# Performance work log

Measured on AMD Instinct MI355X. Metric: run time of the kernel, lower is better.

## Reference

```python
import jax, jax.numpy as jnp
import numpy as np

B, F, C_IN, C_OUT, W_DIM, K2, PAD = 4, 98304, 256, 3, 512, 4, 4096
N = B * F  # total real faces across batch


def setup_inputs() -> dict:
    key = jax.random.key(0)
    ks = jax.random.split(key, 5)
    x = jax.random.normal(ks[0], (N, C_IN), jnp.float32)
    face_neighborhood = jax.random.randint(ks[1], (N, K2), 0, N + PAD)
    # pads placed at the end of the padded slot array (exactly PAD true entries)
    face_is_pad = jnp.concatenate([jnp.zeros((N,), bool), jnp.ones((PAD,), bool)])
    w = jax.random.normal(ks[2], (B, W_DIM), jnp.float32)
    affine_weight = jax.random.normal(ks[3], (C_IN, W_DIM), jnp.float32)
    affine_bias = jnp.ones((C_IN,), jnp.float32)  # bias_init=1
    weight = jax.random.normal(ks[4], (C_OUT, C_IN, 1, K2), jnp.float32)
    bias = jnp.zeros((C_OUT,), jnp.float32)
    return dict(x=x, face_neighborhood=face_neighborhood, face_is_pad=face_is_pad,
                pad_size=PAD, w=w, affine_weight=affine_weight,
                affine_bias=affine_bias, weight=weight, bias=bias)


def reference(x, face_neighborhood, face_is_pad, pad_size, w,
              affine_weight, affine_bias, weight, bias):
    weight_gain = 1.0 / np.sqrt(C_IN * K2)
    # FullyConnectedLayer (stylegan2-ada): out = w @ (A.T / sqrt(in)) + bias(=1)
    styles = (w @ (affine_weight.T / np.float32(np.sqrt(W_DIM))) + affine_bias) * weight_gain  # [B, C_in]
    # create_faceconv_input: scatter real features into padded slots (pads = 0)
    real_rank = jnp.cumsum(~face_is_pad) - 1                      # [N+pad] rank among real slots
    padded = jnp.where(face_is_pad[:, None], jnp.float32(0),
                       x[jnp.clip(real_rank, 0, N - 1)])           # [N+pad, C_in]
    gathered = padded[face_neighborhood]                           # [N, K2, C_in]
    g = gathered.reshape(B, F, K2, C_IN)
    # modulated_face_conv, demodulate=False:
    # out[b,f,o] = sum_{c,k} g[b,f,k,c] * weight[o,c,0,k] * styles[b,c]
    out = jnp.einsum('bfkc,ock,bc->bfo', g, weight[:, :, 0, :], styles)
    out = out.reshape(N, C_OUT) + bias[None, :]
    return jnp.clip(out, -256.0, 256.0)
```

## Files before the change

kernel.cpp:

```cpp
#include <hip/hip_runtime.h>


#define N_FACES   393216
#define C_IN      256
#define C_OUT     3
#define W_DIM     512
#define K2        4
#define BATCH     4
#define F_PER_B   98304
#define NJ        48

typedef __attribute__((ext_vector_type(8))) short bf16x8;
typedef __attribute__((ext_vector_type(4))) float f32x4;

static __device__ __forceinline__ unsigned short f2bf(float f) {
    union { float f; unsigned int u; } v; v.f = f;
    unsigned int r = v.u + 0x7FFFu + ((v.u >> 16) & 1u);
    return (unsigned short)(r >> 16);
}
static __device__ __forceinline__ float bf2f(unsigned short u) {
    union { unsigned int u; float f; } v; v.u = ((unsigned int)u) << 16;
    return v.f;
}

__global__ __launch_bounds__(256) void wmod_bf16_kernel(
    const float* __restrict__ w,
    const float* __restrict__ aw,
    const float* __restrict__ ab,
    const float* __restrict__ weight,
    unsigned short* __restrict__ wmodT)
{
    int t = blockIdx.x * blockDim.x + threadIdx.x;
    if (t >= BATCH * C_IN) return;
    int b = t >> 8;
    int c = t & 255;

    const float* wr = w  + b * W_DIM;
    const float* ar = aw + c * W_DIM;
    float acc = 0.f;
    #pragma unroll 4
    for (int d = 0; d < W_DIM; d += 4) {
        float4 wv = *reinterpret_cast<const float4*>(wr + d);
        float4 av = *reinterpret_cast<const float4*>(ar + d);
        acc += wv.x * av.x + wv.y * av.y + wv.z * av.z + wv.w * av.w;
    }
    const float rsqrt_wdim = 0.04419417382415922f;
    const float gain       = 0.03125f;
    float s = (acc * rsqrt_wdim + ab[c]) * gain;

    #pragma unroll
    for (int o = 0; o < C_OUT; ++o)
        #pragma unroll
        for (int k = 0; k < K2; ++k) {
            int j = b * (K2 * C_OUT) + k * C_OUT + o;
            wmodT[j * C_IN + c] = f2bf(weight[(o * C_IN + c) * K2 + k] * s);
        }
}

#define LDW (C_IN + 8)

__global__ __launch_bounds__(256) void gemm_z_kernel(
    const float*          __restrict__ x,
    const unsigned short* __restrict__ wmodT,
    unsigned short*       __restrict__ z)
{
    __shared__ unsigned short bs[NJ][LDW];

    const unsigned int* g = reinterpret_cast<const unsigned int*>(wmodT);
    for (int i = threadIdx.x; i < NJ * (C_IN / 2); i += 256) {
        int r = i >> 7;
        int c = i & 127;
        reinterpret_cast<unsigned int*>(&bs[r][0])[c] = g[r * 128 + c];
    }
    __syncthreads();

    const int tile = (blockIdx.x * 256 + threadIdx.x) >> 6;
    const int lane = threadIdx.x & 63;
    const int row  = lane & 15;
    const int kq   = lane >> 4;

    const float* xrow = x + (size_t)(tile * 16 + row) * C_IN + kq * 8;

    f32x4 acc0 = {0.f, 0.f, 0.f, 0.f};
    f32x4 acc1 = {0.f, 0.f, 0.f, 0.f};
    f32x4 acc2 = {0.f, 0.f, 0.f, 0.f};

    #pragma unroll
    for (int ks = 0; ks < 8; ++ks) {
        const float4* p = reinterpret_cast<const float4*>(xrow + ks * 32);
        float4 a0 = p[0];
        float4 a1 = p[1];
        union { bf16x8 v; unsigned short u[8]; } af;
        af.u[0] = f2bf(a0.x); af.u[1] = f2bf(a0.y);
        af.u[2] = f2bf(a0.z); af.u[3] = f2bf(a0.w);
        af.u[4] = f2bf(a1.x); af.u[5] = f2bf(a1.y);
        af.u[6] = f2bf(a1.z); af.u[7] = f2bf(a1.w);

        const int cofs = ks * 32 + kq * 8;
        bf16x8 b0 = *reinterpret_cast<const bf16x8*>(&bs[ 0 + row][cofs]);
        bf16x8 b1 = *reinterpret_cast<const bf16x8*>(&bs[16 + row][cofs]);
        bf16x8 b2 = *reinterpret_cast<const bf16x8*>(&bs[32 + row][cofs]);

        acc0 = __builtin_amdgcn_mfma_f32_16x16x32_bf16(af.v, b0, acc0, 0, 0, 0);
        acc1 = __builtin_amdgcn_mfma_f32_16x16x32_bf16(af.v, b1, acc1, 0, 0, 0);
        acc2 = __builtin_amdgcn_mfma_f32_16x16x32_bf16(af.v, b2, acc2, 0, 0, 0);
    }

    const int colj  = lane & 15;
    const int rbase = tile * 16 + kq * 4;
    #pragma unroll
    for (int r = 0; r < 4; ++r) {
        size_t zr = (size_t)(rbase + r) * NJ;
        z[zr +  0 + colj] = f2bf(acc0[r]);
        z[zr + 16 + colj] = f2bf(acc1[r]);
        z[zr + 32 + colj] = f2bf(acc2[r]);
    }
}

__global__ __launch_bounds__(256) void gather_out_kernel(
    const int*            __restrict__ nb,
    const unsigned short* __restrict__ z,
    const float*          __restrict__ bias,
    float*                __restrict__ out)
{
    int n = blockIdx.x * 256 + threadIdx.x;
    if (n >= N_FACES) return;
    int b = n / F_PER_B;

    const int4 idx4 = *reinterpret_cast<const int4*>(nb + n * K2);
    int ids[K2] = { idx4.x, idx4.y, idx4.z, idx4.w };

    float s0 = 0.f, s1 = 0.f, s2 = 0.f;
    #pragma unroll
    for (int k = 0; k < K2; ++k) {
        int id = ids[k];
        if (id < N_FACES) {
            const unsigned short* p = z + (size_t)id * NJ + b * 12 + k * 3;
            s0 += bf2f(p[0]);
            s1 += bf2f(p[1]);
            s2 += bf2f(p[2]);
        }
    }
    s0 = fminf(fmaxf(s0 + bias[0], -256.f), 256.f);
    s1 = fminf(fmaxf(s1 + bias[1], -256.f), 256.f);
    s2 = fminf(fmaxf(s2 + bias[2], -256.f), 256.f);
    float* po = out + (size_t)n * C_OUT;
    po[0] = s0; po[1] = s1; po[2] = s2;
}

__global__ __launch_bounds__(256) void wmod_kernel(
    const float* __restrict__ w, const float* __restrict__ aw,
    const float* __restrict__ ab, const float* __restrict__ weight,
    float* __restrict__ wmod)
{
    int t = blockIdx.x * blockDim.x + threadIdx.x;
    if (t >= BATCH * C_IN) return;
    int b = t >> 8, c = t & 255;
    const float* wr = w + b * W_DIM;
    const float* ar = aw + c * W_DIM;
    float acc = 0.f;
    #pragma unroll 4
    for (int d = 0; d < W_DIM; d += 4) {
        float4 wv = *reinterpret_cast<const float4*>(wr + d);
        float4 av = *reinterpret_cast<const float4*>(ar + d);
        acc += wv.x * av.x + wv.y * av.y + wv.z * av.z + wv.w * av.w;
    }
    float s = (acc * 0.04419417382415922f + ab[c]) * 0.03125f;
    #pragma unroll
    for (int o = 0; o < C_OUT; ++o)
        #pragma unroll
        for (int k = 0; k < K2; ++k)
            wmod[(((b * K2 + k) * C_OUT + o) << 8) + c] =
                weight[(o * C_IN + c) * K2 + k] * s;
}

__global__ __launch_bounds__(256) void face_conv_kernel(
    const float* __restrict__ x, const int* __restrict__ nb,
    const float* __restrict__ wmod, const float* __restrict__ bias,
    float* __restrict__ out)
{
    const int n    = (blockIdx.x * blockDim.x + threadIdx.x) >> 6;
    const int lane = threadIdx.x & 63;
    if (n >= N_FACES) return;
    const int b = n / F_PER_B;
    const int4 idx4 = *reinterpret_cast<const int4*>(nb + n * K2);
    int idx[K2] = { idx4.x, idx4.y, idx4.z, idx4.w };
    const int cofs = lane << 2;
    const float* wm = wmod + ((b * K2 * C_OUT) << 8) + cofs;
    float acc0 = 0.f, acc1 = 0.f, acc2 = 0.f;
    #pragma unroll
    for (int k = 0; k < K2; ++k) {
        const int id = idx[k];
        if (id < N_FACES) {
            const float4 xv = *reinterpret_cast<const float4*>(x + (size_t)id * C_IN + cofs);
            const float* wk = wm + ((k * C_OUT) << 8);
            const float4 w0 = *reinterpret_cast<const float4*>(wk);
            const float4 w1 = *reinterpret_cast<const float4*>(wk + 256);
            const float4 w2 = *reinterpret_cast<const float4*>(wk + 512);
            acc0 += xv.x * w0.x + xv.y * w0.y + xv.z * w0.z + xv.w * w0.w;
            acc1 += xv.x * w1.x + xv.y * w1.y + xv.z * w1.z + xv.w * w1.w;
            acc2 += xv.x * w2.x + xv.y * w2.y + xv.z * w2.z + xv.w * w2.w;
        }
    }
    #pragma unroll
    for (int off = 32; off > 0; off >>= 1) {
        acc0 += __shfl_xor(acc0, off, 64);
        acc1 += __shfl_xor(acc1, off, 64);
        acc2 += __shfl_xor(acc2, off, 64);
    }
    if (lane < C_OUT) {
        float v = (lane == 0) ? acc0 : (lane == 1) ? acc1 : acc2;
        v += bias[lane];
        v = fminf(fmaxf(v, -256.f), 256.f);
        out[n * C_OUT + lane] = v;
    }
}

extern "C" void kernel_launch(void* const* d_in, const int* in_sizes, int n_in,
                              void* d_out, int out_size, void* d_ws, size_t ws_size,
                              hipStream_t stream)
{
    const float* x      = (const float*)d_in[0];
    const int*   nb     = (const int*)  d_in[1];
    const float* w      = (const float*)d_in[4];
    const float* aw     = (const float*)d_in[5];
    const float* ab     = (const float*)d_in[6];
    const float* weight = (const float*)d_in[7];
    const float* bias   = (const float*)d_in[8];
    float*       out    = (float*)d_out;

    const size_t zoff   = 32768;
    const size_t zbytes = (size_t)N_FACES * NJ * sizeof(unsigned short);

    if (ws_size >= zoff + zbytes) {
        unsigned short* wmodT = (unsigned short*)d_ws;
        unsigned short* z     = (unsigned short*)((char*)d_ws + zoff);

        wmod_bf16_kernel<<<(BATCH * C_IN + 255) / 256, 256, 0, stream>>>(
            w, aw, ab, weight, wmodT);

        gemm_z_kernel<<<(N_FACES / 16) / 4, 256, 0, stream>>>(x, wmodT, z);

        gather_out_kernel<<<N_FACES / 256, 256, 0, stream>>>(nb, z, bias, out);
    } else {
        float* wmod = (float*)d_ws;
        wmod_kernel<<<(BATCH * C_IN + 255) / 256, 256, 0, stream>>>(
            w, aw, ab, weight, wmod);
        face_conv_kernel<<<N_FACES / 4, 256, 0, stream>>>(x, nb, wmod, bias, out);
    }
}
```

Measured before the change: 140.7 us.

## Pad z rows to 64 slots with LDS-staged vector stores and 8-byte gathers

Changes the intermediate z layout from 48 packed bf16 per face to 64 slots, so each (batch, k) triple is padded to 4 elements and aligned. The GEMM kernel stages its output tile in shared memory and writes z with 16-byte vector stores instead of scattered 2-byte stores. The gather kernel then reads each neighbour triple with a single 8-byte load instead of three 2-byte loads. The cost is a third more z bytes written and an extra LDS round trip plus barrier. It also switches bf16 conversion to the HIP intrinsic.

```diff
diff --git a/kernel.cpp b/kernel.cpp
--- a/kernel.cpp
+++ b/kernel.cpp
@@ -1,4 +1,5 @@
 #include <hip/hip_runtime.h>
+#include <hip/hip_bf16.h>
 
 
 #define N_FACES   393216
@@ -9,17 +10,13 @@
 #define BATCH     4
 #define F_PER_B   98304
 #define NJ        48
+#define ZSLOTS    64
 
 typedef __attribute__((ext_vector_type(8))) short bf16x8;
 typedef __attribute__((ext_vector_type(4))) float f32x4;
 
-static __device__ __forceinline__ unsigned short f2bf(float f) {
-    union { float f; unsigned int u; } v; v.f = f;
-    unsigned int r = v.u + 0x7FFFu + ((v.u >> 16) & 1u);
-    return (unsigned short)(r >> 16);
-}
-static __device__ __forceinline__ float bf2f(unsigned short u) {
-    union { unsigned int u; float f; } v; v.u = ((unsigned int)u) << 16;
+static __device__ __forceinline__ float bfbits2f(unsigned int hi16) {
+    union { unsigned int u; float f; } v; v.u = hi16;
     return v.f;
 }
 
@@ -53,19 +50,27 @@
         #pragma unroll
         for (int k = 0; k < K2; ++k) {
             int j = b * (K2 * C_OUT) + k * C_OUT + o;
-            wmodT[j * C_IN + c] = f2bf(weight[(o * C_IN + c) * K2 + k] * s);
+            union { __hip_bfloat16 h; unsigned short u; } cv;
+            cv.h = __float2bfloat16(weight[(o * C_IN + c) * K2 + k] * s);
+            wmodT[j * C_IN + c] = cv.u;
         }
 }
 
-#define LDW (C_IN + 8)
+#define LDW 264
 
 __global__ __launch_bounds__(256) void gemm_z_kernel(
     const float*          __restrict__ x,
     const unsigned short* __restrict__ wmodT,
     unsigned short*       __restrict__ z)
 {
-    __shared__ unsigned short bs[NJ][LDW];
-
+    __shared__ __align__(16) unsigned short bs[NJ][LDW];
+    __shared__ __align__(16) unsigned short zs[4][16][ZSLOTS];
+
+    {
+        unsigned int* p = reinterpret_cast<unsigned int*>(&zs[0][0][0]);
+        #pragma unroll
+        for (int i = 0; i < 8; ++i) p[threadIdx.x + 256 * i] = 0u;
+    }
     const unsigned int* g = reinterpret_cast<const unsigned int*>(wmodT);
     for (int i = threadIdx.x; i < NJ * (C_IN / 2); i += 256) {
         int r = i >> 7;
@@ -74,8 +79,9 @@
     }
     __syncthreads();
 
-    const int tile = (blockIdx.x * 256 + threadIdx.x) >> 6;
+    const int wave = threadIdx.x >> 6;
     const int lane = threadIdx.x & 63;
+    const int tile = blockIdx.x * 4 + wave;
     const int row  = lane & 15;
     const int kq   = lane >> 4;
 
@@ -90,11 +96,11 @@
         const float4* p = reinterpret_cast<const float4*>(xrow + ks * 32);
         float4 a0 = p[0];
         float4 a1 = p[1];
-        union { bf16x8 v; unsigned short u[8]; } af;
-        af.u[0] = f2bf(a0.x); af.u[1] = f2bf(a0.y);
-        af.u[2] = f2bf(a0.z); af.u[3] = f2bf(a0.w);
-        af.u[4] = f2bf(a1.x); af.u[5] = f2bf(a1.y);
-        af.u[6] = f2bf(a1.z); af.u[7] = f2bf(a1.w);
+        union { bf16x8 v; __hip_bfloat16 h[8]; } af;
+        af.h[0] = __float2bfloat16(a0.x); af.h[1] = __float2bfloat16(a0.y);
+        af.h[2] = __float2bfloat16(a0.z); af.h[3] = __float2bfloat16(a0.w);
+        af.h[4] = __float2bfloat16(a1.x); af.h[5] = __float2bfloat16(a1.y);
+        af.h[6] = __float2bfloat16(a1.z); af.h[7] = __float2bfloat16(a1.w);
 
         const int cofs = ks * 32 + kq * 8;
         bf16x8 b0 = *reinterpret_cast<const bf16x8*>(&bs[ 0 + row][cofs]);
@@ -106,15 +112,36 @@
         acc2 = __builtin_amdgcn_mfma_f32_16x16x32_bf16(af.v, b2, acc2, 0, 0, 0);
     }
 
-    const int colj  = lane & 15;
-    const int rbase = tile * 16 + kq * 4;
+    const int colj = lane & 15;
+    int slot[3];
+    #pragma unroll
+    for (int a = 0; a < 3; ++a) {
+        int j   = a * 16 + colj;
+        int b   = j / 12;
+        int rem = j - b * 12;
+        slot[a] = b * 16 + rem + rem / 3;
+    }
     #pragma unroll
     for (int r = 0; r < 4; ++r) {
-        size_t zr = (size_t)(rbase + r) * NJ;
-        z[zr +  0 + colj] = f2bf(acc0[r]);
-        z[zr + 16 + colj] = f2bf(acc1[r]);
-        z[zr + 32 + colj] = f2bf(acc2[r]);
-    }
+        const int lr = kq * 4 + r;
+        union { __hip_bfloat16 h; unsigned short u; } c0, c1, c2;
+        c0.h = __float2bfloat16(acc0[r]);
+        c1.h = __float2bfloat16(acc1[r]);
+        c2.h = __float2bfloat16(acc2[r]);
+        zs[wave][lr][slot[0]] = c0.u;
+        zs[wave][lr][slot[1]] = c1.u;
+        zs[wave][lr][slot[2]] = c2.u;
+    }
+    __syncthreads();
+
+    const int rrow = lane >> 2;
+    const int rchk = lane & 3;
+    const uint4* lp = reinterpret_cast<const uint4*>(&zs[wave][rrow][rchk * 16]);
+    uint4 v0 = lp[0];
+    uint4 v1 = lp[1];
+    uint4* zp = reinterpret_cast<uint4*>(z + (size_t)(tile * 16 + rrow) * ZSLOTS + rchk * 16);
+    zp[0] = v0;
+    zp[1] = v1;
 }
 
 __global__ __launch_bounds__(256) void gather_out_kernel(
@@ -135,10 +162,11 @@
     for (int k = 0; k < K2; ++k) {
         int id = ids[k];
         if (id < N_FACES) {
-            const unsigned short* p = z + (size_t)id * NJ + b * 12 + k * 3;
-            s0 += bf2f(p[0]);
-            s1 += bf2f(p[1]);
-            s2 += bf2f(p[2]);
+            uint2 v = *reinterpret_cast<const uint2*>(
+                z + (size_t)id * ZSLOTS + b * 16 + k * 4);
+            s0 += bfbits2f(v.x << 16);
+            s1 += bfbits2f(v.x & 0xffff0000u);
+            s2 += bfbits2f(v.y << 16);
         }
     }
     s0 = fminf(fmaxf(s0 + bias[0], -256.f), 256.f);
@@ -230,7 +258,7 @@
     float*       out    = (float*)d_out;
 
     const size_t zoff   = 32768;
-    const size_t zbytes = (size_t)N_FACES * NJ * sizeof(unsigned short);
+    const size_t zbytes = (size_t)N_FACES * ZSLOTS * sizeof(unsigned short);
 
     if (ws_size >= zoff + zbytes) {
         unsigned short* wmodT = (unsigned short*)d_ws;
```

Result: slower. 144.1 us (+2.4%).
